# Kernel optimization log

Measured on AMD Instinct MI355X. Metric: run time of the kernel, lower is better.

## Reference

```python
import jax, jax.numpy as jnp
import numpy as np

B, DIM, RES, NS, ITERS = 64, 256, 32, 8, 5
NTOK = RES * RES
HID = max(DIM, 128)
EPS = 1e-08
SCALE = DIM ** -0.5


def build_grid(res):
    r = [np.linspace(0.0, 1.0, num=n) for n in (res, res)]
    g = np.stack(np.meshgrid(*r, sparse=False, indexing='ij'), axis=-1)
    g = g.reshape(1, res, res, 2).astype(np.float32)
    return jnp.asarray(np.concatenate([g, 1.0 - g], axis=-1))  # [1,res,res,4]


def ln(x, g, b, eps=1e-5):
    m = x.mean(-1, keepdims=True)
    v = ((x - m) ** 2).mean(-1, keepdims=True)
    return (x - m) / jnp.sqrt(v + eps) * g + b


def ln2(x, g, b, eps=1e-5):  # LayerNorm over last two dims ([ntokens, dim])
    m = x.mean((-2, -1), keepdims=True)
    v = ((x - m) ** 2).mean((-2, -1), keepdims=True)
    return (x - m) / jnp.sqrt(v + eps) * g + b


def lin(x, W, b):
    return x @ W.T + b


def gru_cell(x, h, W_ih, W_hh, b_ih, b_hh):
    gi = x @ W_ih.T + b_ih
    gh = h @ W_hh.T + b_hh
    ir, iz, i_n = jnp.split(gi, 3, axis=-1)
    hr, hz, h_n = jnp.split(gh, 3, axis=-1)
    r = jax.nn.sigmoid(ir + hr)
    z = jax.nn.sigmoid(iz + hz)
    n = jnp.tanh(i_n + r * h_n)
    return (1.0 - z) * n + z * h


def setup_inputs() -> dict:
    key = jax.random.key(0)
    ks = jax.random.split(key, 32)
    p = lambda i, shape, s=0.02: (jax.random.normal(ks[i], shape, dtype=jnp.float32) * s)
    d = {
        'inputs': jax.random.normal(ks[0], (B, DIM, RES, RES), dtype=jnp.float32),
        'init_noise': jax.random.normal(ks[1], (B, NS, DIM), dtype=jnp.float32),
        'W_pos': p(2, (DIM, 4)), 'b_pos': jnp.zeros((DIM,)),
        'g_enc': jnp.ones((NTOK, DIM)), 'b_enc': jnp.zeros((NTOK, DIM)),
        'W_m1': p(3, (DIM, DIM)), 'b_m1': jnp.zeros((DIM,)),
        'W_m2': p(4, (DIM, DIM)), 'b_m2': jnp.zeros((DIM,)),
        'g_in': jnp.ones((DIM,)), 'b_in': jnp.zeros((DIM,)),
        'Wq': p(5, (DIM, DIM)), 'bq': jnp.zeros((DIM,)),
        'Wk': p(6, (DIM, DIM)), 'bk': jnp.zeros((DIM,)),
        'Wv': p(7, (DIM, DIM)), 'bv': jnp.zeros((DIM,)),
        'W_ih': p(8, (3 * DIM, DIM)), 'W_hh': p(9, (3 * DIM, DIM)),
        'b_ih': jnp.zeros((3 * DIM,)), 'b_hh': jnp.zeros((3 * DIM,)),
        'g_s': jnp.ones((DIM,)), 'b_s': jnp.zeros((DIM,)),
        'g_ff': jnp.ones((DIM,)), 'b_ff': jnp.zeros((DIM,)),
        'W_f1': p(10, (HID, DIM)), 'b_f1': jnp.zeros((HID,)),
        'W_f2': p(11, (DIM, HID)), 'b_f2': jnp.zeros((DIM,)),
        'mu': p(12, (1, 1, DIM), 0.1), 'sigma': p(13, (1, 1, DIM), 0.1),
    }
    return d


def _forward(inputs, init_noise, W_pos, b_pos, g_enc, b_enc, W_m1, b_m1, W_m2, b_m2,
             g_in, b_in, Wq, bq, Wk, bk, Wv, bv, W_ih, W_hh, b_ih, b_hh,
             g_s, b_s, g_ff, b_ff, W_f1, b_f1, W_f2, b_f2, mu, sigma):
    grid = build_grid(RES)  # [1,RES,RES,4]
    # encoder transformation (position=True)
    f = jnp.transpose(inputs, (0, 2, 3, 1))               # [B,RES,RES,DIM]
    f = f + lin(grid, W_pos, b_pos)                       # soft position embed
    f = f.reshape(B, NTOK, DIM)
    f = ln2(f, g_enc, b_enc)                              # LayerNorm([ntokens, dim])
    f = jnp.maximum(lin(f, W_m1, b_m1), 0.0)
    f = jnp.maximum(lin(f, W_m2, b_m2), 0.0)
    f = ln(f, g_in, b_in)                                 # norm_input
    k = lin(f, Wk, bk)
    v = lin(f, Wv, bv)

    def step(slots):
        s = ln(slots, g_s, b_s)
        q = lin(s, Wq, bq)
        dots = jnp.einsum('bid,bjd->bij', q, k) * SCALE   # [B,NS,NTOK]
        attn = jax.nn.softmax(dots, axis=1) + EPS         # softmax over slots
        attn = attn / attn.sum(-1, keepdims=True)         # weighted mean
        upd = jnp.einsum('bij,bjd->bid', attn, v)
        ns = gru_cell(upd.reshape(-1, DIM), slots.reshape(-1, DIM),
                      W_ih, W_hh, b_ih, b_hh).reshape(B, NS, DIM)
        h = jnp.maximum(lin(ln(ns, g_ff, b_ff), W_f1, b_f1), 0.0)
        return ns + lin(h, W_f2, b_f2)

    slots = mu + sigma * init_noise
    for _ in range(ITERS):
        slots = step(slots)
    # implicit differentiation: one extra step through detached slots
    slots = step(jax.lax.stop_gradient(slots))
    return slots


def reference(inputs, init_noise, W_pos, b_pos, g_enc, b_enc, W_m1, b_m1, W_m2, b_m2,
              g_in, b_in, Wq, bq, Wk, bk, Wv, bv, W_ih, W_hh, b_ih, b_hh,
              g_s, b_s, g_ff, b_ff, W_f1, b_f1, W_f2, b_f2, mu, sigma):
    return _forward(inputs, init_noise, W_pos, b_pos, g_enc, b_enc, W_m1, b_m1, W_m2, b_m2,
                    g_in, b_in, Wq, bq, Wk, bk, Wv, bv, W_ih, W_hh, b_ih, b_hh,
                    g_s, b_s, g_ff, b_ff, W_f1, b_f1, W_f2, b_f2, mu, sigma)
```

## Files before the change

kernel.cpp:

```cpp
#include <hip/hip_runtime.h>
#include <hip/hip_bf16.h>

#define BB    64
#define DIMN  256
#define NSLOT 8
#define NTOKN 1024
#define NSTEP 6
#define SCALEF 0.0625f

typedef __attribute__((ext_vector_type(8))) short short8;
typedef __attribute__((ext_vector_type(8))) unsigned short ushort8;
typedef __attribute__((ext_vector_type(4))) unsigned short ushort4v;
typedef __attribute__((ext_vector_type(4))) float f32x4;

__device__ __forceinline__ float b2f(unsigned short u) {
  return __uint_as_float((unsigned)u << 16);
}
__device__ __forceinline__ unsigned short f2b(float f) {
  unsigned u = __float_as_uint(f);
  return (unsigned short)((u + 0x7FFFu + ((u >> 16) & 1u)) >> 16);
}

constexpr int kNConv = 31;
constexpr int kConvSizes[kNConv] = {
  131072, 1024, 256, 262144, 262144, 65536, 256, 65536, 256, 256, 256,
  65536, 256, 65536, 256, 65536, 256, 196608, 196608, 768, 768,
  256, 256, 256, 256, 65536, 256, 65536, 256, 256, 256
};
constexpr int kConvTotal = 1513984;

struct PtrPack { const void* p[kNConv]; };

__device__ __forceinline__ float ldin(const void* p, long i, int isbf) {
  if (isbf) return b2f(((const unsigned short*)p)[i]);
  return ((const float*)p)[i];
}

__global__ void detect_dtype(const void* gin, int* flag) {
  unsigned u = *(const unsigned*)gin;
  *flag = (u == 0x3F803F80u) ? 1 : 0;
}

__global__ __launch_bounds__(256) void convert_weights(PtrPack pk, const int* __restrict__ flag,
                                                       float* __restrict__ dst) {
  int idx = blockIdx.x * 256 + threadIdx.x;
  if (idx >= kConvTotal) return;
  int off = idx, a = 0;
  while (a < kNConv - 1 && off >= kConvSizes[a]) { off -= kConvSizes[a]; ++a; }
  dst[idx] = ldin(pk.p[a], off, *flag);
}

constexpr int kWN = 9;
constexpr int kWSize[kWN]  = {65536, 65536, 65536, 65536, 65536, 196608, 196608, 65536, 65536};
constexpr int kWSrc[kWN]   = {656640, 722432, 788736, 854528, 920320, 986112, 1182720, 1381888, 1447680};
constexpr int kWTotal = 851968;

__global__ __launch_bounds__(256) void convert_wbf16(const float* __restrict__ conv,
                                                     unsigned short* __restrict__ wbf) {
  int idx = blockIdx.x * 256 + threadIdx.x;
  if (idx >= kWTotal) return;
  int off = idx, m = 0;
  while (m < kWN - 1 && off >= kWSize[m]) { off -= kWSize[m]; ++m; }
  wbf[idx] = f2b(conv[kWSrc[m] + off]);
}

__global__ __launch_bounds__(256) void posembed_stats(
    const void* __restrict__ in0, const int* __restrict__ flag,
    const float* __restrict__ Wpos, const float* __restrict__ bpos,
    unsigned short* __restrict__ A, float* __restrict__ partials) {
  __shared__ float lds[64 * 65];
  __shared__ float red[8];
  const int tb = blockIdx.x, b = blockIdx.y, tid = threadIdx.x;
  const int t0 = tb * 64;
  const int isbf = *flag;
  float sum = 0.f, ss = 0.f;
  const int tg = tid & 7;
  const int dbase = tid >> 3;
  const int tloc = tg * 8;
  const int dq = tid & 15;
  const int trow = tid >> 4;
  for (int d0 = 0; d0 < DIMN; d0 += 64) {
    __syncthreads();
#pragma unroll
    for (int p = 0; p < 2; ++p) {
      int dd = dbase + p * 32;
      int d = d0 + dd;
      const float* wp = Wpos + d * 4;
      int tf = t0 + tloc;
      float gi = (float)(tf >> 5) * (1.f / 31.f);
      float gj0 = (float)(tf & 31) * (1.f / 31.f);
      float base = wp[0] * gi + wp[2] * (1.f - gi) + wp[1] * gj0 + wp[3] * (1.f - gj0) + bpos[d];
      float step = (wp[1] - wp[3]) * (1.f / 31.f);
      long gidx = ((long)b * DIMN + d) * NTOKN + tf;
      float v[8];
      if (isbf) {
        ushort8 raw = *(const ushort8*)((const unsigned short*)in0 + gidx);
#pragma unroll
        for (int j = 0; j < 8; ++j) v[j] = b2f(raw[j]);
      } else {
        const float* fp = (const float*)in0 + gidx;
        float4 a0 = *(const float4*)fp;
        float4 a1 = *(const float4*)(fp + 4);
        v[0] = a0.x; v[1] = a0.y; v[2] = a0.z; v[3] = a0.w;
        v[4] = a1.x; v[5] = a1.y; v[6] = a1.z; v[7] = a1.w;
      }
#pragma unroll
      for (int j = 0; j < 8; ++j) {
        float val = v[j] + base + step * (float)j;
        sum += val; ss += val * val;
        lds[dd * 65 + tloc + j] = val;
      }
    }
    __syncthreads();
#pragma unroll
    for (int p = 0; p < 4; ++p) {
      int tt = trow + p * 16;
      int dcol = dq * 4;
      ushort4v y;
      y[0] = f2b(lds[(dcol + 0) * 65 + tt]);
      y[1] = f2b(lds[(dcol + 1) * 65 + tt]);
      y[2] = f2b(lds[(dcol + 2) * 65 + tt]);
      y[3] = f2b(lds[(dcol + 3) * 65 + tt]);
      *(ushort4v*)(A + ((long)b * NTOKN + t0 + tt) * DIMN + d0 + dcol) = y;
    }
  }
  for (int off = 32; off; off >>= 1) { sum += __shfl_xor(sum, off); ss += __shfl_xor(ss, off); }
  int w = tid >> 6;
  if ((tid & 63) == 0) { red[w] = sum; red[4 + w] = ss; }
  __syncthreads();
  if (tid == 0) {
    partials[((long)b * 16 + tb) * 2]     = red[0] + red[1] + red[2] + red[3];
    partials[((long)b * 16 + tb) * 2 + 1] = red[4] + red[5] + red[6] + red[7];
  }
}

__global__ void stats_reduce(const float* __restrict__ partials, float* __restrict__ stats) {
  int b = threadIdx.x;
  if (b >= BB) return;
  float s = 0.f, q = 0.f;
  for (int i = 0; i < 16; ++i) {
    s += partials[((long)b * 16 + i) * 2];
    q += partials[((long)b * 16 + i) * 2 + 1];
  }
  const float invN = 1.f / (float)(NTOKN * DIMN);
  float m = s * invN;
  float var = q * invN - m * m;
  stats[b * 2] = m;
  stats[b * 2 + 1] = rsqrtf(var + 1e-5f);
}

__global__ __launch_bounds__(512) void gemm_m1ln(
    const unsigned short* __restrict__ X, const float* __restrict__ stats,
    const float* __restrict__ genc, const float* __restrict__ benc,
    const unsigned short* __restrict__ W, const float* __restrict__ bias,
    unsigned short* __restrict__ Y) {
  __shared__ unsigned short As[128 * 264];
  __shared__ unsigned short Bs[128 * 264];
  const int tid = threadIdx.x;
  const long m0 = (long)blockIdx.x * 128;
  const int n0 = blockIdx.y * 128;
  const int bb_ = (int)(m0 >> 10);
  const float mm = stats[bb_ * 2], inv = stats[bb_ * 2 + 1];
#pragma unroll
  for (int i = 0; i < 8; ++i) {
    int c = tid + i * 512;
    int row = c >> 5, seg = c & 31;
    long grow = m0 + row;
    int t = (int)(grow & 1023);
    ushort8 raw = *(const ushort8*)(X + grow * 256 + seg * 8);
    const float* gp = genc + (long)t * 256 + seg * 8;
    const float* bp = benc + (long)t * 256 + seg * 8;
    ushort8 y;
#pragma unroll
    for (int e = 0; e < 8; ++e)
      y[e] = f2b((b2f(raw[e]) - mm) * inv * gp[e] + bp[e]);
    *(ushort8*)&As[row * 264 + seg * 8] = y;
  }
#pragma unroll
  for (int i = 0; i < 8; ++i) {
    int c = tid + i * 512;
    int row = c >> 5, seg = c & 31;
    *(ushort8*)&Bs[row * 264 + seg * 8] = *(const ushort8*)(W + (long)(n0 + row) * 256 + seg * 8);
  }
  __syncthreads();
  const int wave = tid >> 6, lane = tid & 63;
  const int wr = wave >> 1, wc = wave & 1;
  const int lrow = lane & 15, kgrp = lane >> 4;
  f32x4 acc[2][4];
#pragma unroll
  for (int mt = 0; mt < 2; ++mt)
#pragma unroll
    for (int nt = 0; nt < 4; ++nt) acc[mt][nt] = f32x4{0.f, 0.f, 0.f, 0.f};
#pragma unroll
  for (int kc = 0; kc < 8; ++kc) {
    short8 af[2], bf[4];
#pragma unroll
    for (int mt = 0; mt < 2; ++mt)
      af[mt] = *(const short8*)&As[(wr * 32 + mt * 16 + lrow) * 264 + kc * 32 + kgrp * 8];
#pragma unroll
    for (int nt = 0; nt < 4; ++nt)
      bf[nt] = *(const short8*)&Bs[(wc * 64 + nt * 16 + lrow) * 264 + kc * 32 + kgrp * 8];
#pragma unroll
    for (int mt = 0; mt < 2; ++mt)
#pragma unroll
      for (int nt = 0; nt < 4; ++nt)
        acc[mt][nt] = __builtin_amdgcn_mfma_f32_16x16x32_bf16(af[mt], bf[nt], acc[mt][nt], 0, 0, 0);
  }
#pragma unroll
  for (int mt = 0; mt < 2; ++mt)
#pragma unroll
    for (int nt = 0; nt < 4; ++nt) {
      int n = n0 + wc * 64 + nt * 16 + lrow;
      float bn = bias[n];
#pragma unroll
      for (int r = 0; r < 4; ++r) {
        long m = m0 + wr * 32 + mt * 16 + kgrp * 4 + r;
        Y[m * 256 + n] = f2b(fmaxf(acc[mt][nt][r] + bn, 0.f));
      }
    }
}

template <int ACT, int OUT>
__global__ __launch_bounds__(512) void gemm_tile(
    const unsigned short* __restrict__ X, const unsigned short* __restrict__ W,
    const float* __restrict__ bias, const float* __restrict__ res,
    void* __restrict__ Y, int Nfull) {
  __shared__ unsigned short As[128 * 264];
  __shared__ unsigned short Bs[128 * 264];
  const int tid = threadIdx.x;
  const long m0 = (long)blockIdx.x * 128;
  const int n0 = blockIdx.y * 128;
#pragma unroll
  for (int i = 0; i < 8; ++i) {
    int c = tid + i * 512;
    int row = c >> 5, seg = c & 31;
    *(ushort8*)&As[row * 264 + seg * 8] = *(const ushort8*)(X + (m0 + row) * 256 + seg * 8);
  }
#pragma unroll
  for (int i = 0; i < 8; ++i) {
    int c = tid + i * 512;
    int row = c >> 5, seg = c & 31;
    *(ushort8*)&Bs[row * 264 + seg * 8] = *(const ushort8*)(W + (long)(n0 + row) * 256 + seg * 8);
  }
  __syncthreads();
  const int wave = tid >> 6, lane = tid & 63;
  const int wr = wave >> 1, wc = wave & 1;
  const int lrow = lane & 15, kgrp = lane >> 4;
  f32x4 acc[2][4];
#pragma unroll
  for (int mt = 0; mt < 2; ++mt)
#pragma unroll
    for (int nt = 0; nt < 4; ++nt) acc[mt][nt] = f32x4{0.f, 0.f, 0.f, 0.f};
#pragma unroll
  for (int kc = 0; kc < 8; ++kc) {
    short8 af[2], bf[4];
#pragma unroll
    for (int mt = 0; mt < 2; ++mt)
      af[mt] = *(const short8*)&As[(wr * 32 + mt * 16 + lrow) * 264 + kc * 32 + kgrp * 8];
#pragma unroll
    for (int nt = 0; nt < 4; ++nt)
      bf[nt] = *(const short8*)&Bs[(wc * 64 + nt * 16 + lrow) * 264 + kc * 32 + kgrp * 8];
#pragma unroll
    for (int mt = 0; mt < 2; ++mt)
#pragma unroll
      for (int nt = 0; nt < 4; ++nt)
        acc[mt][nt] = __builtin_amdgcn_mfma_f32_16x16x32_bf16(af[mt], bf[nt], acc[mt][nt], 0, 0, 0);
  }
#pragma unroll
  for (int mt = 0; mt < 2; ++mt)
#pragma unroll
    for (int nt = 0; nt < 4; ++nt) {
      int n = n0 + wc * 64 + nt * 16 + lrow;
      float bn = bias[n];
#pragma unroll
      for (int r = 0; r < 4; ++r) {
        long m = m0 + wr * 32 + mt * 16 + kgrp * 4 + r;
        float v = acc[mt][nt][r] + bn;
        if (ACT) v = fmaxf(v, 0.f);
        if (OUT == 0)      ((unsigned short*)Y)[m * Nfull + n] = f2b(v);
        else if (OUT == 1) ((float*)Y)[m * Nfull + n] = v;
        else               ((float*)Y)[m * Nfull + n] = v + res[m * Nfull + n];
      }
    }
}

__global__ __launch_bounds__(512) void gemm_kv_tile(
    const unsigned short* __restrict__ X,
    const float* __restrict__ gin, const float* __restrict__ bin,
    const unsigned short* __restrict__ Wk, const unsigned short* __restrict__ Wv,
    const float* __restrict__ bk, const float* __restrict__ bv,
    unsigned short* __restrict__ Kb, unsigned short* __restrict__ Vb) {
  __shared__ unsigned short As[128 * 264];
  __shared__ unsigned short Bs[128 * 264];
  const int tid = threadIdx.x;
  const long m0 = (long)blockIdx.x * 128;
  const int n0 = blockIdx.y * 128;
#pragma unroll
  for (int i = 0; i < 8; ++i) {
    int c = tid + i * 512;
    int row = c >> 5, seg = c & 31;
    ushort8 raw = *(const ushort8*)(X + (m0 + row) * 256 + seg * 8);
    float v[8];
    float s = 0.f, q = 0.f;
#pragma unroll
    for (int e = 0; e < 8; ++e) {
      v[e] = b2f(raw[e]);
      s += v[e]; q += v[e] * v[e];
    }
#pragma unroll
    for (int msk = 1; msk <= 16; msk <<= 1) {
      s += __shfl_xor(s, msk);
      q += __shfl_xor(q, msk);
    }
    float mean = s * (1.f / 256.f);
    float rinv = rsqrtf(q * (1.f / 256.f) - mean * mean + 1e-5f);
    const float* gp = gin + seg * 8;
    const float* bp = bin + seg * 8;
    ushort8 y;
#pragma unroll
    for (int e = 0; e < 8; ++e)
      y[e] = f2b((v[e] - mean) * rinv * gp[e] + bp[e]);
    *(ushort8*)&As[row * 264 + seg * 8] = y;
  }
  const int wave = tid >> 6, lane = tid & 63;
  const int wr = wave >> 1, wc = wave & 1;
  const int lrow = lane & 15, kgrp = lane >> 4;
  for (int which = 0; which < 2; ++which) {
    const unsigned short* W = which ? Wv : Wk;
    const float* bias = which ? bv : bk;
    unsigned short* Y = which ? Vb : Kb;
    if (which) __syncthreads();
#pragma unroll
    for (int i = 0; i < 8; ++i) {
      int c = tid + i * 512;
      int row = c >> 5, seg = c & 31;
      *(ushort8*)&Bs[row * 264 + seg * 8] = *(const ushort8*)(W + (long)(n0 + row) * 256 + seg * 8);
    }
    __syncthreads();
    f32x4 acc[2][4];
#pragma unroll
    for (int mt = 0; mt < 2; ++mt)
#pragma unroll
      for (int nt = 0; nt < 4; ++nt) acc[mt][nt] = f32x4{0.f, 0.f, 0.f, 0.f};
#pragma unroll
    for (int kc = 0; kc < 8; ++kc) {
      short8 af[2], bf[4];
#pragma unroll
      for (int mt = 0; mt < 2; ++mt)
        af[mt] = *(const short8*)&As[(wr * 32 + mt * 16 + lrow) * 264 + kc * 32 + kgrp * 8];
#pragma unroll
      for (int nt = 0; nt < 4; ++nt)
        bf[nt] = *(const short8*)&Bs[(wc * 64 + nt * 16 + lrow) * 264 + kc * 32 + kgrp * 8];
#pragma unroll
      for (int mt = 0; mt < 2; ++mt)
#pragma unroll
        for (int nt = 0; nt < 4; ++nt)
          acc[mt][nt] = __builtin_amdgcn_mfma_f32_16x16x32_bf16(af[mt], bf[nt], acc[mt][nt], 0, 0, 0);
    }
#pragma unroll
    for (int mt = 0; mt < 2; ++mt)
#pragma unroll
      for (int nt = 0; nt < 4; ++nt) {
        int n = n0 + wc * 64 + nt * 16 + lrow;
        float bn = bias[n];
#pragma unroll
        for (int r = 0; r < 4; ++r) {
          long m = m0 + wr * 32 + mt * 16 + kgrp * 4 + r;
          Y[m * 256 + n] = f2b(acc[mt][nt][r] + bn);
        }
      }
  }
}

template <int ACT, int OUT>
__global__ __launch_bounds__(256) void gemm_tile64(
    const unsigned short* __restrict__ X, const unsigned short* __restrict__ W,
    const float* __restrict__ bias, const float* __restrict__ res,
    void* __restrict__ Y, int Nfull) {
  __shared__ unsigned short As[64 * 264];
  __shared__ unsigned short Bs[128 * 264];
  const int tid = threadIdx.x;
  const long m0 = (long)blockIdx.x * 64;
  const int n0 = blockIdx.y * 128;
#pragma unroll
  for (int i = 0; i < 8; ++i) {
    int c = tid + i * 256;
    int row = c >> 5, seg = c & 31;
    *(ushort8*)&As[row * 264 + seg * 8] = *(const ushort8*)(X + (m0 + row) * 256 + seg * 8);
  }
#pragma unroll
  for (int i = 0; i < 16; ++i) {
    int c = tid + i * 256;
    int row = c >> 5, seg = c & 31;
    *(ushort8*)&Bs[row * 264 + seg * 8] = *(const ushort8*)(W + (long)(n0 + row) * 256 + seg * 8);
  }
  __syncthreads();
  const int wave = tid >> 6, lane = tid & 63;
  const int lrow = lane & 15, kgrp = lane >> 4;
  f32x4 acc[8];
#pragma unroll
  for (int nt = 0; nt < 8; ++nt) acc[nt] = f32x4{0.f, 0.f, 0.f, 0.f};
#pragma unroll
  for (int kc = 0; kc < 8; ++kc) {
    short8 af = *(const short8*)&As[(wave * 16 + lrow) * 264 + kc * 32 + kgrp * 8];
#pragma unroll
    for (int nt = 0; nt < 8; ++nt) {
      short8 bf = *(const short8*)&Bs[(nt * 16 + lrow) * 264 + kc * 32 + kgrp * 8];
      acc[nt] = __builtin_amdgcn_mfma_f32_16x16x32_bf16(af, bf, acc[nt], 0, 0, 0);
    }
  }
#pragma unroll
  for (int nt = 0; nt < 8; ++nt) {
    int n = n0 + nt * 16 + lrow;
    float bn = bias[n];
#pragma unroll
    for (int r = 0; r < 4; ++r) {
      long m = m0 + wave * 16 + kgrp * 4 + r;
      float v = acc[nt][r] + bn;
      if (ACT) v = fmaxf(v, 0.f);
      if (OUT == 0)      ((unsigned short*)Y)[m * Nfull + n] = f2b(v);
      else if (OUT == 1) ((float*)Y)[m * Nfull + n] = v;
      else               ((float*)Y)[m * Nfull + n] = v + res[m * Nfull + n];
    }
  }
}

__global__ __launch_bounds__(512) void gigh_tile(
    const unsigned short* __restrict__ updb, const unsigned short* __restrict__ sbf,
    const unsigned short* __restrict__ Wih, const unsigned short* __restrict__ Whh,
    const float* __restrict__ bih, const float* __restrict__ bhh,
    float* __restrict__ gib, float* __restrict__ ghb) {
  const unsigned short* X = blockIdx.z ? sbf : updb;
  const unsigned short* W = blockIdx.z ? Whh : Wih;
  const float* bias = blockIdx.z ? bhh : bih;
  float* Y = blockIdx.z ? ghb : gib;
  __shared__ unsigned short As[128 * 264];
  __shared__ unsigned short Bs[128 * 264];
  const int tid = threadIdx.x;
  const long m0 = (long)blockIdx.x * 128;
  const int n0 = blockIdx.y * 128;
#pragma unroll
  for (int i = 0; i < 8; ++i) {
    int c = tid + i * 512;
    int row = c >> 5, seg = c & 31;
    *(ushort8*)&As[row * 264 + seg * 8] = *(const ushort8*)(X + (m0 + row) * 256 + seg * 8);
  }
#pragma unroll
  for (int i = 0; i < 8; ++i) {
    int c = tid + i * 512;
    int row = c >> 5, seg = c & 31;
    *(ushort8*)&Bs[row * 264 + seg * 8] = *(const ushort8*)(W + (long)(n0 + row) * 256 + seg * 8);
  }
  __syncthreads();
  const int wave = tid >> 6, lane = tid & 63;
  const int wr = wave >> 1, wc = wave & 1;
  const int lrow = lane & 15, kgrp = lane >> 4;
  f32x4 acc[2][4];
#pragma unroll
  for (int mt = 0; mt < 2; ++mt)
#pragma unroll
    for (int nt = 0; nt < 4; ++nt) acc[mt][nt] = f32x4{0.f, 0.f, 0.f, 0.f};
#pragma unroll
  for (int kc = 0; kc < 8; ++kc) {
    short8 af[2], bf[4];
#pragma unroll
    for (int mt = 0; mt < 2; ++mt)
      af[mt] = *(const short8*)&As[(wr * 32 + mt * 16 + lrow) * 264 + kc * 32 + kgrp * 8];
#pragma unroll
    for (int nt = 0; nt < 4; ++nt)
      bf[nt] = *(const short8*)&Bs[(wc * 64 + nt * 16 + lrow) * 264 + kc * 32 + kgrp * 8];
#pragma unroll
    for (int mt = 0; mt < 2; ++mt)
#pragma unroll
      for (int nt = 0; nt < 4; ++nt)
        acc[mt][nt] = __builtin_amdgcn_mfma_f32_16x16x32_bf16(af[mt], bf[nt], acc[mt][nt], 0, 0, 0);
  }
#pragma unroll
  for (int mt = 0; mt < 2; ++mt)
#pragma unroll
    for (int nt = 0; nt < 4; ++nt) {
      int n = n0 + wc * 64 + nt * 16 + lrow;
      float bn = bias[n];
#pragma unroll
      for (int r = 0; r < 4; ++r) {
        long m = m0 + wr * 32 + mt * 16 + kgrp * 4 + r;
        Y[m * 768 + n] = acc[mt][nt][r] + bn;
      }
    }
}

__global__ __launch_bounds__(256) void slots_init(const float* __restrict__ noise, const float* __restrict__ mu,
                                                  const float* __restrict__ sigma, float* __restrict__ slots) {
  long i = (long)blockIdx.x * 256 + threadIdx.x;
  int d = (int)(i & 255);
  slots[i] = mu[d] + sigma[d] * noise[i];
}

__global__ __launch_bounds__(256) void lnq_q(
    const float* __restrict__ slots, const float* __restrict__ gs, const float* __restrict__ bs,
    const unsigned short* __restrict__ Wq, const float* __restrict__ bq,
    unsigned short* __restrict__ qb, unsigned short* __restrict__ sbf) {
  __shared__ unsigned short S[16 * 264];
  const int b = blockIdx.x, tid = threadIdx.x;
  const int wave = tid >> 6, lane = tid & 63;
  for (int i = tid; i < 8 * 264; i += 256) S[8 * 264 + i] = 0;
#pragma unroll
  for (int rr = 0; rr < 2; ++rr) {
    int row = wave * 2 + rr;
    float4 xv = *(const float4*)(slots + ((long)b * 8 + row) * 256 + lane * 4);
    float s = xv.x + xv.y + xv.z + xv.w;
    float q = xv.x * xv.x + xv.y * xv.y + xv.z * xv.z + xv.w * xv.w;
    for (int off = 32; off; off >>= 1) { s += __shfl_xor(s, off); q += __shfl_xor(q, off); }
    float m = s * (1.f / 256.f);
    float inv = rsqrtf(q * (1.f / 256.f) - m * m + 1e-5f);
    float4 gv = *(const float4*)(gs + lane * 4);
    float4 bv = *(const float4*)(bs + lane * 4);
    ushort4v y, rb;
    y[0] = f2b((xv.x - m) * inv * gv.x + bv.x);
    y[1] = f2b((xv.y - m) * inv * gv.y + bv.y);
    y[2] = f2b((xv.z - m) * inv * gv.z + bv.z);
    y[3] = f2b((xv.w - m) * inv * gv.w + bv.w);
    rb[0] = f2b(xv.x); rb[1] = f2b(xv.y); rb[2] = f2b(xv.z); rb[3] = f2b(xv.w);
    *(ushort4v*)&S[row * 264 + lane * 4] = y;
    *(ushort4v*)(sbf + ((long)b * 8 + row) * 256 + lane * 4) = rb;
  }
  __syncthreads();
  const int lrow = lane & 15, kgrp = lane >> 4;
  short8 a[8];
#pragma unroll
  for (int kc = 0; kc < 8; ++kc)
    a[kc] = *(const short8*)&S[lrow * 264 + kc * 32 + kgrp * 8];
#pragma unroll
  for (int nt = 0; nt < 4; ++nt) {
    const int n = wave * 64 + nt * 16 + lrow;
    const unsigned short* wp = Wq + (long)n * 256 + kgrp * 8;
    f32x4 acc = {0.f, 0.f, 0.f, 0.f};
#pragma unroll
    for (int kc = 0; kc < 8; ++kc)
      acc = __builtin_amdgcn_mfma_f32_16x16x32_bf16(a[kc], *(const short8*)(wp + kc * 32), acc, 0, 0, 0);
    if (kgrp < 2) {
      float bn = bq[n];
#pragma unroll
      for (int r = 0; r < 4; ++r)
        qb[((long)b * 8 + kgrp * 4 + r) * 256 + n] = f2b(acc[r] + bn);
    }
  }
}

__global__ __launch_bounds__(256) void attn1b(
    const unsigned short* __restrict__ qb, const unsigned short* __restrict__ Kb,
    const unsigned short* __restrict__ Vb,
    unsigned short* __restrict__ upd_part, float* __restrict__ asum_part) {
  __shared__ unsigned short Ks[64 * 264];
  __shared__ unsigned short Qs[16 * 264];
  __shared__ float attnS[64 * 8];
  __shared__ float red[4 * 2048];
  const int jt = blockIdx.x, b = blockIdx.y, tid = threadIdx.x;
  const int wave = tid >> 6, lane = tid & 63;
#pragma unroll
  for (int i = 0; i < 8; ++i) {
    int c = tid + i * 256;
    int row = c >> 5, seg = c & 31;
    *(ushort8*)&Ks[row * 264 + seg * 8] =
        *(const ushort8*)(Kb + ((long)(b * NTOKN + jt * 64 + row)) * 256 + seg * 8);
  }
  {
    int row = tid >> 5, seg = tid & 31;
    *(ushort8*)&Qs[row * 264 + seg * 8] = *(const ushort8*)(qb + ((long)(b * 8 + row)) * 256 + seg * 8);
  }
  for (int i = tid; i < 8 * 264; i += 256) Qs[8 * 264 + i] = 0;
  __syncthreads();
  const int lrow = lane & 15, kgrp = lane >> 4;
  f32x4 acc = {0.f, 0.f, 0.f, 0.f};
#pragma unroll
  for (int kc = 0; kc < 8; ++kc) {
    short8 af = *(const short8*)&Ks[(wave * 16 + lrow) * 264 + kc * 32 + kgrp * 8];
    short8 qf = *(const short8*)&Qs[lrow * 264 + kc * 32 + kgrp * 8];
    acc = __builtin_amdgcn_mfma_f32_16x16x32_bf16(af, qf, acc, 0, 0, 0);
  }
  float t0[4], mx[4], e[4], sm[4];
#pragma unroll
  for (int r = 0; r < 4; ++r) { t0[r] = acc[r] * SCALEF; mx[r] = t0[r]; }
#pragma unroll
  for (int msk = 1; msk <= 4; msk <<= 1)
#pragma unroll
    for (int r = 0; r < 4; ++r) mx[r] = fmaxf(mx[r], __shfl_xor(mx[r], msk));
#pragma unroll
  for (int r = 0; r < 4; ++r) { e[r] = expf(t0[r] - mx[r]); sm[r] = e[r]; }
#pragma unroll
  for (int msk = 1; msk <= 4; msk <<= 1)
#pragma unroll
    for (int r = 0; r < 4; ++r) sm[r] += __shfl_xor(sm[r], msk);
  if (lrow < 8) {
#pragma unroll
    for (int r = 0; r < 4; ++r) {
      int jl = wave * 16 + kgrp * 4 + r;
      attnS[jl * 8 + lrow] = e[r] / sm[r] + 1e-8f;
    }
  }
  __syncthreads();
  {
    int s0 = wave * 2;
    float v0 = attnS[lane * 8 + s0], v1 = attnS[lane * 8 + s0 + 1];
    for (int off = 32; off; off >>= 1) { v0 += __shfl_xor(v0, off); v1 += __shfl_xor(v1, off); }
    if (lane == 0) {
      asum_part[((long)(b * 16 + jt)) * 8 + s0] = v0;
      asum_part[((long)(b * 16 + jt)) * 8 + s0 + 1] = v1;
    }
  }
  float au[8][4] = {};
  for (int jl = 0; jl < 16; ++jl) {
    int j = wave * 16 + jl;
    ushort4v v4 = *(const ushort4v*)(Vb + ((long)(b * NTOKN + jt * 64 + j)) * 256 + lane * 4);
    float v0 = b2f(v4[0]), v1 = b2f(v4[1]), v2 = b2f(v4[2]), v3 = b2f(v4[3]);
    float4 a01 = *(const float4*)&attnS[j * 8];
    float4 a23 = *(const float4*)&attnS[j * 8 + 4];
    float aw[8] = {a01.x, a01.y, a01.z, a01.w, a23.x, a23.y, a23.z, a23.w};
#pragma unroll
    for (int s = 0; s < 8; ++s) {
      au[s][0] += aw[s] * v0; au[s][1] += aw[s] * v1;
      au[s][2] += aw[s] * v2; au[s][3] += aw[s] * v3;
    }
  }
#pragma unroll
  for (int s = 0; s < 8; ++s)
    *(float4*)&red[wave * 2048 + s * 256 + lane * 4] = make_float4(au[s][0], au[s][1], au[s][2], au[s][3]);
  __syncthreads();
#pragma unroll
  for (int i = 0; i < 8; ++i) {
    int idx = tid + i * 256;
    float sum = red[idx] + red[2048 + idx] + red[4096 + idx] + red[6144 + idx];
    upd_part[((long)(b * 16 + jt)) * 2048 + idx] = f2b(sum);
  }
}

__global__ __launch_bounds__(256) void upd_reduce(
    const unsigned short* __restrict__ upd_part, const float* __restrict__ asum_part,
    unsigned short* __restrict__ updb) {
  const int bx = blockIdx.x;
  const int b = bx >> 3, s = bx & 7;
  const int tid = threadIdx.x;
  float as = 0.f;
#pragma unroll
  for (int jt = 0; jt < 16; ++jt) as += asum_part[((long)(b * 16 + jt)) * 8 + s];
  float sum = 0.f;
#pragma unroll
  for (int jt = 0; jt < 16; ++jt)
    sum += b2f(upd_part[((long)(b * 16 + jt)) * 2048 + s * 256 + tid]);
  updb[((long)b * 8 + s) * 256 + tid] = f2b(sum / as);
}

__global__ __launch_bounds__(256) void gru_ln(const float* __restrict__ gi, const float* __restrict__ gh,
                                              const float* __restrict__ slots,
                                              const float* __restrict__ gff, const float* __restrict__ bff,
                                              float* __restrict__ ns, unsigned short* __restrict__ ffl) {
  const int tid = threadIdx.x, lane = tid & 63;
  const long row = (long)blockIdx.x * 4 + (tid >> 6);
  const int d = lane * 4;
  float4 i1 = *(const float4*)(gi + row * 768 + d);
  float4 i2 = *(const float4*)(gi + row * 768 + 256 + d);
  float4 i3 = *(const float4*)(gi + row * 768 + 512 + d);
  float4 h1 = *(const float4*)(gh + row * 768 + d);
  float4 h2 = *(const float4*)(gh + row * 768 + 256 + d);
  float4 h3 = *(const float4*)(gh + row * 768 + 512 + d);
  float4 sl = *(const float4*)(slots + row * 256 + d);
  float n4[4];
  float r, z, nn;
  r = 1.f / (1.f + expf(-(i1.x + h1.x))); z = 1.f / (1.f + expf(-(i2.x + h2.x)));
  nn = tanhf(i3.x + r * h3.x); n4[0] = (1.f - z) * nn + z * sl.x;
  r = 1.f / (1.f + expf(-(i1.y + h1.y))); z = 1.f / (1.f + expf(-(i2.y + h2.y)));
  nn = tanhf(i3.y + r * h3.y); n4[1] = (1.f - z) * nn + z * sl.y;
  r = 1.f / (1.f + expf(-(i1.z + h1.z))); z = 1.f / (1.f + expf(-(i2.z + h2.z)));
  nn = tanhf(i3.z + r * h3.z); n4[2] = (1.f - z) * nn + z * sl.z;
  r = 1.f / (1.f + expf(-(i1.w + h1.w))); z = 1.f / (1.f + expf(-(i2.w + h2.w)));
  nn = tanhf(i3.w + r * h3.w); n4[3] = (1.f - z) * nn + z * sl.w;
  *(float4*)(ns + row * 256 + d) = make_float4(n4[0], n4[1], n4[2], n4[3]);
  float s = n4[0] + n4[1] + n4[2] + n4[3];
  float q = n4[0] * n4[0] + n4[1] * n4[1] + n4[2] * n4[2] + n4[3] * n4[3];
  for (int off = 32; off; off >>= 1) { s += __shfl_xor(s, off); q += __shfl_xor(q, off); }
  float m = s * (1.f / 256.f);
  float inv = rsqrtf(q * (1.f / 256.f) - m * m + 1e-5f);
  float4 gv = *(const float4*)(gff + d);
  float4 bv = *(const float4*)(bff + d);
  ushort4v y;
  y[0] = f2b((n4[0] - m) * inv * gv.x + bv.x);
  y[1] = f2b((n4[1] - m) * inv * gv.y + bv.y);
  y[2] = f2b((n4[2] - m) * inv * gv.z + bv.z);
  y[3] = f2b((n4[3] - m) * inv * gv.w + bv.w);
  *(ushort4v*)(ffl + row * 256 + d) = y;
}

__global__ __launch_bounds__(256) void write_out(const float* __restrict__ slots, const int* __restrict__ flag,
                                                 void* __restrict__ out) {
  long i = (long)blockIdx.x * 256 + threadIdx.x;
  float v = slots[i];
  if (*flag) ((__hip_bfloat16*)out)[i] = __float2bfloat16(v);
  else ((float*)out)[i] = v;
}

extern "C" void kernel_launch(void* const* d_in, const int* in_sizes, int n_in,
                              void* d_out, int out_size, void* d_ws, size_t ws_size,
                              hipStream_t stream) {
  (void)in_sizes; (void)n_in; (void)out_size; (void)ws_size;
  float* wsf = (float*)d_ws;
  long o = 0;
  float* conv = wsf; o += kConvTotal;
  unsigned short* wbf = (unsigned short*)(wsf + o); o += kWTotal / 2;
  unsigned short* A   = (unsigned short*)(wsf + o); o += (long)BB * NTOKN * DIMN / 2;
  unsigned short* X1  = (unsigned short*)(wsf + o); o += (long)BB * NTOKN * DIMN / 2;
  unsigned short* X2  = (unsigned short*)(wsf + o); o += (long)BB * NTOKN * DIMN / 2;
  unsigned short* Kb  = (unsigned short*)(wsf + o); o += (long)BB * NTOKN * DIMN / 2;
  unsigned short* Vb  = (unsigned short*)(wsf + o); o += (long)BB * NTOKN * DIMN / 2;
  float* slots = wsf + o; o += 131072;
  unsigned short* sbf = (unsigned short*)(wsf + o); o += 65536;
  unsigned short* qb  = (unsigned short*)(wsf + o); o += 65536;
  unsigned short* upd_part = (unsigned short*)(wsf + o); o += 1048576;
  float* asum_part = wsf + o; o += 8192;
  unsigned short* updb = (unsigned short*)(wsf + o); o += 65536;
  float* gib   = wsf + o; o += 393216;
  float* ghb   = wsf + o; o += 393216;
  float* nsb   = wsf + o; o += 131072;
  unsigned short* ffl  = (unsigned short*)(wsf + o); o += 65536;
  unsigned short* hbuf = (unsigned short*)(wsf + o); o += 65536;
  float* partials = wsf + o; o += 2048;
  float* stats = wsf + o; o += 128;
  int* flag = (int*)(wsf + o); o += 16;

  long coff[kNConv];
  { long acc = 0; for (int i = 0; i < kNConv; ++i) { coff[i] = acc; acc += kConvSizes[i]; } }
  const float* noise_f = conv + coff[0];
  const float* Wpos = conv + coff[1];
  const float* bpos = conv + coff[2];
  const float* genc = conv + coff[3];
  const float* benc = conv + coff[4];
  const float* bm1  = conv + coff[6];
  const float* bm2  = conv + coff[8];
  const float* gin  = conv + coff[9];
  const float* bin  = conv + coff[10];
  const float* bq   = conv + coff[12];
  const float* bk   = conv + coff[14];
  const float* bv   = conv + coff[16];
  const float* bih  = conv + coff[19];
  const float* bhh  = conv + coff[20];
  const float* gs   = conv + coff[21];
  const float* bs   = conv + coff[22];
  const float* gff  = conv + coff[23];
  const float* bff  = conv + coff[24];
  const float* bf1  = conv + coff[26];
  const float* bf2  = conv + coff[28];
  const float* mu   = conv + coff[29];
  const float* sigma = conv + coff[30];

  const unsigned short* Wm1b = wbf;
  const unsigned short* Wm2b = wbf + 65536;
  const unsigned short* Wqb  = wbf + 131072;
  const unsigned short* Wkb  = wbf + 196608;
  const unsigned short* Wvb  = wbf + 262144;
  const unsigned short* Wihb = wbf + 327680;
  const unsigned short* Whhb = wbf + 524288;
  const unsigned short* Wf1b = wbf + 720896;
  const unsigned short* Wf2b = wbf + 786432;

  detect_dtype<<<1, 1, 0, stream>>>(d_in[10], flag);

  PtrPack pk;
  for (int i = 0; i < kNConv; ++i) pk.p[i] = d_in[i + 1];
  convert_weights<<<(kConvTotal + 255) / 256, 256, 0, stream>>>(pk, flag, conv);
  convert_wbf16<<<(kWTotal + 255) / 256, 256, 0, stream>>>(conv, wbf);

  posembed_stats<<<dim3(16, 64), 256, 0, stream>>>(d_in[0], flag, Wpos, bpos, A, partials);
  stats_reduce<<<1, 64, 0, stream>>>(partials, stats);
  const int MT = BB * NTOKN / 128;
  gemm_m1ln<<<dim3(MT, 2), 512, 0, stream>>>(A, stats, genc, benc, Wm1b, bm1, X1);
  gemm_tile<1, 0><<<dim3(MT, 2), 512, 0, stream>>>(X1, Wm2b, bm2, nullptr, X2, 256);
  gemm_kv_tile<<<dim3(MT, 2), 512, 0, stream>>>(X2, gin, bin, Wkb, Wvb, bk, bv, Kb, Vb);

  slots_init<<<512, 256, 0, stream>>>(noise_f, mu, sigma, slots);

  for (int it = 0; it < NSTEP; ++it) {
    lnq_q<<<64, 256, 0, stream>>>(slots, gs, bs, Wqb, bq, qb, sbf);
    attn1b<<<dim3(16, 64), 256, 0, stream>>>(qb, Kb, Vb, upd_part, asum_part);
    upd_reduce<<<512, 256, 0, stream>>>(upd_part, asum_part, updb);
    gigh_tile<<<dim3(4, 6, 2), 512, 0, stream>>>(updb, sbf, Wihb, Whhb, bih, bhh, gib, ghb);
    gru_ln<<<128, 256, 0, stream>>>(gib, ghb, slots, gff, bff, nsb, ffl);
    gemm_tile64<1, 0><<<dim3(8, 2), 256, 0, stream>>>(ffl, Wf1b, bf1, nullptr, hbuf, 256);
    gemm_tile64<0, 2><<<dim3(8, 2), 256, 0, stream>>>(hbuf, Wf2b, bf2, nsb, slots, 256);
  }

  write_out<<<512, 256, 0, stream>>>(slots, flag, d_out);
}
```

Baseline: 404.0 us.

## Fuse slot LayerNorm and Q projection into attention kernel; emit bf16 slots from FFN epilogue

Removes the separate lnq_q launch in each iteration. Every attention block now recomputes the LayerNorm and Q projection for its batch in shared memory instead of reading Q from global memory. The bf16 copy of the slots is written by slots_init and by the FFN residual epilogue instead. This saves one launch and a global round trip per step, at the cost of recomputing Q in 16 blocks per batch: extra MFMA work plus reads of Wq, and more shared memory per block.

```diff
diff --git a/kernel.cpp b/kernel.cpp
--- a/kernel.cpp
+++ b/kernel.cpp
@@ -376,7 +376,7 @@
 __global__ __launch_bounds__(256) void gemm_tile64(
     const unsigned short* __restrict__ X, const unsigned short* __restrict__ W,
     const float* __restrict__ bias, const float* __restrict__ res,
-    void* __restrict__ Y, int Nfull) {
+    void* __restrict__ Y, unsigned short* __restrict__ sbout, int Nfull) {
   __shared__ unsigned short As[64 * 264];
   __shared__ unsigned short Bs[128 * 264];
   const int tid = threadIdx.x;
@@ -420,7 +420,12 @@
       if (ACT) v = fmaxf(v, 0.f);
       if (OUT == 0)      ((unsigned short*)Y)[m * Nfull + n] = f2b(v);
       else if (OUT == 1) ((float*)Y)[m * Nfull + n] = v;
-      else               ((float*)Y)[m * Nfull + n] = v + res[m * Nfull + n];
+      else if (OUT == 2) ((float*)Y)[m * Nfull + n] = v + res[m * Nfull + n];
+      else {
+        float o = v + res[m * Nfull + n];
+        ((float*)Y)[m * Nfull + n] = o;
+        sbout[m * Nfull + n] = f2b(o);
+      }
     }
   }
 }
@@ -490,20 +495,35 @@
 }
 
 __global__ __launch_bounds__(256) void slots_init(const float* __restrict__ noise, const float* __restrict__ mu,
-                                                  const float* __restrict__ sigma, float* __restrict__ slots) {
+                                                  const float* __restrict__ sigma, float* __restrict__ slots,
+                                                  unsigned short* __restrict__ sbf) {
   long i = (long)blockIdx.x * 256 + threadIdx.x;
   int d = (int)(i & 255);
-  slots[i] = mu[d] + sigma[d] * noise[i];
-}
-
-__global__ __launch_bounds__(256) void lnq_q(
+  float v = mu[d] + sigma[d] * noise[i];
+  slots[i] = v;
+  sbf[i] = f2b(v);
+}
+
+__global__ __launch_bounds__(256) void attn1b(
     const float* __restrict__ slots, const float* __restrict__ gs, const float* __restrict__ bs,
     const unsigned short* __restrict__ Wq, const float* __restrict__ bq,
-    unsigned short* __restrict__ qb, unsigned short* __restrict__ sbf) {
+    const unsigned short* __restrict__ Kb, const unsigned short* __restrict__ Vb,
+    unsigned short* __restrict__ upd_part, float* __restrict__ asum_part) {
+  __shared__ unsigned short Ks[64 * 264];
+  __shared__ unsigned short Qs[16 * 264];
   __shared__ unsigned short S[16 * 264];
-  const int b = blockIdx.x, tid = threadIdx.x;
+  __shared__ float attnS[64 * 8];
+  __shared__ float red[4 * 2048];
+  const int jt = blockIdx.x, b = blockIdx.y, tid = threadIdx.x;
   const int wave = tid >> 6, lane = tid & 63;
-  for (int i = tid; i < 8 * 264; i += 256) S[8 * 264 + i] = 0;
+#pragma unroll
+  for (int i = 0; i < 8; ++i) {
+    int c = tid + i * 256;
+    int row = c >> 5, seg = c & 31;
+    *(ushort8*)&Ks[row * 264 + seg * 8] =
+        *(const ushort8*)(Kb + ((long)(b * NTOKN + jt * 64 + row)) * 256 + seg * 8);
+  }
+  for (int i = tid; i < 8 * 264; i += 256) { S[8 * 264 + i] = 0; Qs[8 * 264 + i] = 0; }
 #pragma unroll
   for (int rr = 0; rr < 2; ++rr) {
     int row = wave * 2 + rr;
@@ -515,62 +535,37 @@
     float inv = rsqrtf(q * (1.f / 256.f) - m * m + 1e-5f);
     float4 gv = *(const float4*)(gs + lane * 4);
     float4 bv = *(const float4*)(bs + lane * 4);
-    ushort4v y, rb;
+    ushort4v y;
     y[0] = f2b((xv.x - m) * inv * gv.x + bv.x);
     y[1] = f2b((xv.y - m) * inv * gv.y + bv.y);
     y[2] = f2b((xv.z - m) * inv * gv.z + bv.z);
     y[3] = f2b((xv.w - m) * inv * gv.w + bv.w);
-    rb[0] = f2b(xv.x); rb[1] = f2b(xv.y); rb[2] = f2b(xv.z); rb[3] = f2b(xv.w);
     *(ushort4v*)&S[row * 264 + lane * 4] = y;
-    *(ushort4v*)(sbf + ((long)b * 8 + row) * 256 + lane * 4) = rb;
   }
   __syncthreads();
   const int lrow = lane & 15, kgrp = lane >> 4;
-  short8 a[8];
-#pragma unroll
-  for (int kc = 0; kc < 8; ++kc)
-    a[kc] = *(const short8*)&S[lrow * 264 + kc * 32 + kgrp * 8];
-#pragma unroll
-  for (int nt = 0; nt < 4; ++nt) {
-    const int n = wave * 64 + nt * 16 + lrow;
-    const unsigned short* wp = Wq + (long)n * 256 + kgrp * 8;
-    f32x4 acc = {0.f, 0.f, 0.f, 0.f};
+  {
+    short8 a[8];
 #pragma unroll
     for (int kc = 0; kc < 8; ++kc)
-      acc = __builtin_amdgcn_mfma_f32_16x16x32_bf16(a[kc], *(const short8*)(wp + kc * 32), acc, 0, 0, 0);
-    if (kgrp < 2) {
-      float bn = bq[n];
-#pragma unroll
-      for (int r = 0; r < 4; ++r)
-        qb[((long)b * 8 + kgrp * 4 + r) * 256 + n] = f2b(acc[r] + bn);
-    }
-  }
-}
-
-__global__ __launch_bounds__(256) void attn1b(
-    const unsigned short* __restrict__ qb, const unsigned short* __restrict__ Kb,
-    const unsigned short* __restrict__ Vb,
-    unsigned short* __restrict__ upd_part, float* __restrict__ asum_part) {
-  __shared__ unsigned short Ks[64 * 264];
-  __shared__ unsigned short Qs[16 * 264];
-  __shared__ float attnS[64 * 8];
-  __shared__ float red[4 * 2048];
-  const int jt = blockIdx.x, b = blockIdx.y, tid = threadIdx.x;
-  const int wave = tid >> 6, lane = tid & 63;
-#pragma unroll
-  for (int i = 0; i < 8; ++i) {
-    int c = tid + i * 256;
-    int row = c >> 5, seg = c & 31;
-    *(ushort8*)&Ks[row * 264 + seg * 8] =
-        *(const ushort8*)(Kb + ((long)(b * NTOKN + jt * 64 + row)) * 256 + seg * 8);
-  }
-  {
-    int row = tid >> 5, seg = tid & 31;
-    *(ushort8*)&Qs[row * 264 + seg * 8] = *(const ushort8*)(qb + ((long)(b * 8 + row)) * 256 + seg * 8);
-  }
-  for (int i = tid; i < 8 * 264; i += 256) Qs[8 * 264 + i] = 0;
-  __syncthreads();
-  const int lrow = lane & 15, kgrp = lane >> 4;
+      a[kc] = *(const short8*)&S[lrow * 264 + kc * 32 + kgrp * 8];
+#pragma unroll
+    for (int nt = 0; nt < 4; ++nt) {
+      const int n = wave * 64 + nt * 16 + lrow;
+      const unsigned short* wp = Wq + (long)n * 256 + kgrp * 8;
+      f32x4 acc = {0.f, 0.f, 0.f, 0.f};
+#pragma unroll
+      for (int kc = 0; kc < 8; ++kc)
+        acc = __builtin_amdgcn_mfma_f32_16x16x32_bf16(a[kc], *(const short8*)(wp + kc * 32), acc, 0, 0, 0);
+      if (kgrp < 2) {
+        float bn = bq[n];
+#pragma unroll
+        for (int r = 0; r < 4; ++r)
+          Qs[(kgrp * 4 + r) * 264 + n] = f2b(acc[r] + bn);
+      }
+    }
+  }
+  __syncthreads();
   f32x4 acc = {0.f, 0.f, 0.f, 0.f};
 #pragma unroll
   for (int kc = 0; kc < 8; ++kc) {
@@ -713,7 +708,6 @@
   unsigned short* Vb  = (unsigned short*)(wsf + o); o += (long)BB * NTOKN * DIMN / 2;
   float* slots = wsf + o; o += 131072;
   unsigned short* sbf = (unsigned short*)(wsf + o); o += 65536;
-  unsigned short* qb  = (unsigned short*)(wsf + o); o += 65536;
   unsigned short* upd_part = (unsigned short*)(wsf + o); o += 1048576;
   float* asum_part = wsf + o; o += 8192;
   unsigned short* updb = (unsigned short*)(wsf + o); o += 65536;
@@ -775,16 +769,15 @@
   gemm_tile<1, 0><<<dim3(MT, 2), 512, 0, stream>>>(X1, Wm2b, bm2, nullptr, X2, 256);
   gemm_kv_tile<<<dim3(MT, 2), 512, 0, stream>>>(X2, gin, bin, Wkb, Wvb, bk, bv, Kb, Vb);
 
-  slots_init<<<512, 256, 0, stream>>>(noise_f, mu, sigma, slots);
+  slots_init<<<512, 256, 0, stream>>>(noise_f, mu, sigma, slots, sbf);
 
   for (int it = 0; it < NSTEP; ++it) {
-    lnq_q<<<64, 256, 0, stream>>>(slots, gs, bs, Wqb, bq, qb, sbf);
-    attn1b<<<dim3(16, 64), 256, 0, stream>>>(qb, Kb, Vb, upd_part, asum_part);
+    attn1b<<<dim3(16, 64), 256, 0, stream>>>(slots, gs, bs, Wqb, bq, Kb, Vb, upd_part, asum_part);
     upd_reduce<<<512, 256, 0, stream>>>(upd_part, asum_part, updb);
     gigh_tile<<<dim3(4, 6, 2), 512, 0, stream>>>(updb, sbf, Wihb, Whhb, bih, bhh, gib, ghb);
     gru_ln<<<128, 256, 0, stream>>>(gib, ghb, slots, gff, bff, nsb, ffl);
-    gemm_tile64<1, 0><<<dim3(8, 2), 256, 0, stream>>>(ffl, Wf1b, bf1, nullptr, hbuf, 256);
-    gemm_tile64<0, 2><<<dim3(8, 2), 256, 0, stream>>>(hbuf, Wf2b, bf2, nsb, slots, 256);
+    gemm_tile64<1, 0><<<dim3(8, 2), 256, 0, stream>>>(ffl, Wf1b, bf1, nullptr, hbuf, nullptr, 256);
+    gemm_tile64<0, 3><<<dim3(8, 2), 256, 0, stream>>>(hbuf, Wf2b, bf2, nsb, slots, sbf, 256);
   }
 
   write_out<<<512, 256, 0, stream>>>(slots, flag, d_out);
```

Measured after the change: 521.9 us. 1.29x slower.
